# Kernel optimization log

Hardware: AMD Instinct MI355X
Metric: run time of the kernel (lower is better)

## Reference

```python
import jax, jax.numpy as jnp
import numpy as np

N, M, D = 4096, 8192, 512

def setup_inputs() -> dict:
    key = jax.random.key(0)
    k1, k2, k3, k4 = jax.random.split(key, 4)
    X = jax.random.normal(k1, (N, D), dtype=jnp.float32)
    SV = jax.random.normal(k2, (M, D), dtype=jnp.float32)
    DC = jax.random.normal(k3, (1, M), dtype=jnp.float32)
    IC = jax.random.normal(k4, (1,), dtype=jnp.float32)
    gamma = jnp.float32(1.0 / D)
    return {"X": X, "SV": SV, "DC": DC, "IC": IC, "gamma": gamma}

def reference(X, SV, DC, IC, gamma):
    # Squared pairwise L2 distances via GEMM expansion (same math as
    # ||SV - x||^2 without materializing the [N, M, D] broadcast tensor):
    # d2[n, m] = ||x_n||^2 + ||sv_m||^2 - 2 * x_n . sv_m
    x2 = jnp.sum(X * X, axis=1)          # [N]
    sv2 = jnp.sum(SV * SV, axis=1)       # [M]
    cross = jnp.einsum("nd,md->nm", X, SV)  # [N, M]
    d2 = jnp.maximum(x2[:, None] + sv2[None, :] - 2.0 * cross, 0.0)
    k = jnp.exp(-gamma * d2)             # RBF kernel values [N, M]
    # Weighted reduction over support vectors + intercept -> decision values [N]
    return jnp.sum(k * DC, axis=1) + IC
```

## Files before the change

kernel.cpp:

```cpp
#include <hip/hip_runtime.h>
#include <stdint.h>

#define NN 4096
#define MM 8192
#define DD 512
#define KT 8

typedef __bf16 bf16x8 __attribute__((ext_vector_type(8)));
typedef float f32x4 __attribute__((ext_vector_type(4)));
typedef float f32x16 __attribute__((ext_vector_type(16)));

__device__ __forceinline__ void load_lds16(const void* g, void* l) {
  __builtin_amdgcn_global_load_lds(
      (const __attribute__((address_space(1))) unsigned int*)g,
      (__attribute__((address_space(3))) unsigned int*)l, 16, 0, 0);
}

template <int CTRL>
__device__ __forceinline__ float dpp_radd(float x) {
  int xi = __float_as_int(x);
  int mv = __builtin_amdgcn_update_dpp(xi, xi, CTRL, 0xF, 0xF, false);
  return x + __int_as_float(mv);
}
__device__ __forceinline__ float swz_add_xor16(float x) {
  int sv = __builtin_amdgcn_ds_swizzle(__float_as_int(x), 0x401F);
  return x + __int_as_float(sv);
}

__global__ __launch_bounds__(256) void convert_norm_kernel(
    const float* __restrict__ X, const float* __restrict__ SV,
    bf16x8* __restrict__ Xf, bf16x8* __restrict__ SVb,
    float* __restrict__ x2, float* __restrict__ sv2,
    float* __restrict__ out, const float* __restrict__ IC) {
  int wid = blockIdx.x * 4 + (threadIdx.x >> 6);
  int lane = threadIdx.x & 63;
  const float* src;
  float* nrm;
  bool isX = (wid < NN);
  int r = isX ? wid : wid - NN;
  if (isX) {
    src = X + (size_t)r * DD;
    nrm = x2 + r;
    if (lane == 0) out[r] = IC[0];
  } else {
    src = SV + (size_t)r * DD;
    nrm = sv2 + r;
  }
  const f32x4* s = (const f32x4*)src;
  f32x4 a = s[2 * lane];
  f32x4 b = s[2 * lane + 1];
  float sum = a.x * a.x + a.y * a.y + a.z * a.z + a.w * a.w +
              b.x * b.x + b.y * b.y + b.z * b.z + b.w * b.w;
  bf16x8 o;
  o[0] = (__bf16)a.x; o[1] = (__bf16)a.y; o[2] = (__bf16)a.z; o[3] = (__bf16)a.w;
  o[4] = (__bf16)b.x; o[5] = (__bf16)b.y; o[6] = (__bf16)b.z; o[7] = (__bf16)b.w;
  if (isX) {
    const int rg = r >> 5, r31 = r & 31;
    Xf[((size_t)(rg * 32 + (lane >> 1))) * 64 + (lane & 1) * 32 + r31] = o;
  } else {
    SVb[(size_t)r * 64 + lane] = o;
  }
#pragma unroll
  for (int m = 32; m >= 1; m >>= 1) sum += __shfl_xor(sum, m, 64);
  if (lane == 0) *nrm = sum;
}

__global__ __launch_bounds__(256, 4) void rbf_gemm_kernel(
    const bf16x8* __restrict__ Xf, const bf16x8* __restrict__ SVb,
    const float* __restrict__ x2, const float* __restrict__ sv2,
    const float* __restrict__ DC, const float* __restrict__ gamma_p,
    float* __restrict__ out) {
  __shared__ bf16x8 Bs[2][1024];

  const int t = threadIdx.x;
  const int lane = t & 63;
  const int wave = t >> 6;
  const int n0 = blockIdx.x * 128;
  const int m0 = blockIdx.y * 128;

  const int wave_m = wave & 1;
  const int wave_n = wave >> 1;
  const int l31 = lane & 31;
  const int lhi = lane >> 5;

  const int srow = t >> 3;
  const int sslot = t & 7;

  const int rgb = blockIdx.x * 4 + wave_n * 2;
  const bf16x8* a0p = Xf + (size_t)rgb * 2048 + lane;
  const bf16x8* a1p = a0p + 2048;

  f32x16 acc[2][2];
#pragma unroll
  for (int i = 0; i < 2; ++i)
#pragma unroll
    for (int j = 0; j < 2; ++j)
#pragma unroll
      for (int r = 0; r < 16; ++r) acc[i][j][r] = 0.0f;

#pragma unroll
  for (int it = 0; it < 4; ++it) {
    const int c = it * 256 + t;
    const int row = it * 32 + srow;
    const int kg = sslot ^ (row & 7);
    load_lds16(SVb + (size_t)(m0 + row) * 64 + kg, &Bs[0][c]);
  }
  __syncthreads();

#pragma unroll
  for (int kt = 0; kt < KT; ++kt) {
    const int cur = kt & 1;
    const int nxt = cur ^ 1;
    if (kt + 1 < KT) {
#pragma unroll
      for (int it = 0; it < 4; ++it) {
        const int c = it * 256 + t;
        const int row = it * 32 + srow;
        const int kg = sslot ^ (row & 7);
        load_lds16(SVb + (size_t)(m0 + row) * 64 + (kt + 1) * 8 + kg,
                   &Bs[nxt][c]);
      }
    }
#pragma unroll
    for (int ks = 0; ks < 4; ++ks) {
      const int sg = kt * 4 + ks;
      bf16x8 af0 = a0p[(size_t)sg * 64];
      bf16x8 af1 = a1p[(size_t)sg * 64];
      const int kc = ks * 2 + lhi;
      const int sw = kc ^ (l31 & 7);
      const int rb = (wave_m * 64 + l31) * 8;
      bf16x8 bf0 = Bs[cur][rb + sw];
      bf16x8 bf1 = Bs[cur][rb + 256 + sw];
      acc[0][0] = __builtin_amdgcn_mfma_f32_32x32x16_bf16(af0, bf0, acc[0][0], 0, 0, 0);
      acc[0][1] = __builtin_amdgcn_mfma_f32_32x32x16_bf16(af0, bf1, acc[0][1], 0, 0, 0);
      acc[1][0] = __builtin_amdgcn_mfma_f32_32x32x16_bf16(af1, bf0, acc[1][0], 0, 0, 0);
      acc[1][1] = __builtin_amdgcn_mfma_f32_32x32x16_bf16(af1, bf1, acc[1][1], 0, 0, 0);
    }
    __syncthreads();
  }

  const float g = gamma_p[0];
  const float c2 = g * 1.4426950408889634f;

  float sv2v[2], dcv[2];
  const int colb = m0 + wave_m * 64 + l31;
  sv2v[0] = sv2[colb];
  dcv[0] = DC[colb];
  sv2v[1] = sv2[colb + 32];
  dcv[1] = DC[colb + 32];

#pragma unroll
  for (int i = 0; i < 2; ++i) {
    const int rowb = n0 + wave_n * 64 + i * 32 + 4 * lhi;
    float val[16];
#pragma unroll
    for (int g4 = 0; g4 < 4; ++g4) {
      f32x4 xv = *(const f32x4*)(x2 + rowb + 8 * g4);
#pragma unroll
      for (int r2 = 0; r2 < 4; ++r2) {
        const int reg = g4 * 4 + r2;
        float v = 0.0f;
#pragma unroll
        for (int j = 0; j < 2; ++j) {
          float d2 = xv[r2] + sv2v[j] - 2.0f * acc[i][j][reg];
          d2 = fmaxf(d2, 0.0f);
          v += exp2f(-c2 * d2) * dcv[j];
        }
        val[reg] = v;
      }
    }
#pragma unroll
    for (int reg = 0; reg < 16; ++reg) {
      float v = val[reg];
      v = dpp_radd<0x121>(v);
      v = dpp_radd<0x122>(v);
      v = dpp_radd<0x124>(v);
      v = dpp_radd<0x128>(v);
      val[reg] = swz_add_xor16(v);
    }
    if (l31 == 0) {
#pragma unroll
      for (int g4 = 0; g4 < 4; ++g4)
#pragma unroll
        for (int r2 = 0; r2 < 4; ++r2)
          atomicAdd(&out[rowb + 8 * g4 + r2], val[g4 * 4 + r2]);
    }
  }
}

extern "C" void kernel_launch(void* const* d_in, const int* in_sizes, int n_in,
                              void* d_out, int out_size, void* d_ws, size_t ws_size,
                              hipStream_t stream) {
  const float* X = (const float*)d_in[0];
  const float* SV = (const float*)d_in[1];
  const float* DC = (const float*)d_in[2];
  const float* IC = (const float*)d_in[3];
  const float* gamma = (const float*)d_in[4];
  float* out = (float*)d_out;

  char* ws = (char*)d_ws;
  bf16x8* Xf = (bf16x8*)ws;
  bf16x8* SVb = (bf16x8*)(ws + (size_t)NN * DD * 2);
  float* x2 = (float*)(ws + (size_t)(NN + MM) * DD * 2);
  float* sv2 = x2 + NN;

  convert_norm_kernel<<<(NN + MM) / 4, 256, 0, stream>>>(X, SV, Xf, SVb, x2, sv2, out, IC);
  dim3 grid(NN / 128, MM / 128);
  rbf_gemm_kernel<<<grid, 256, 0, stream>>>(Xf, SVb, x2, sv2, DC, gamma, out);
}
```

Baseline: 140.6 us.

## Load SV fragments directly from global in MFMA layout, drop LDS staging

SV is now converted into the same fragment-major layout as X, so each wave loads both MFMA operands straight from global memory with register double-buffering. The LDS tile, swizzle and per-stage barriers are removed. Occupancy hint drops from 4 to 3 blocks to leave room for the extra registers. The cost is that each B fragment is fetched by two waves instead of once per block through LDS, which doubles global/L2 traffic for B.

Result: slower. 150.1 us (+6.8%).

```diff
diff --git a/kernel.cpp b/kernel.cpp
--- a/kernel.cpp
+++ b/kernel.cpp
@@ -4,17 +4,10 @@
 #define NN 4096
 #define MM 8192
 #define DD 512
-#define KT 8
 
 typedef __bf16 bf16x8 __attribute__((ext_vector_type(8)));
 typedef float f32x4 __attribute__((ext_vector_type(4)));
 typedef float f32x16 __attribute__((ext_vector_type(16)));
-
-__device__ __forceinline__ void load_lds16(const void* g, void* l) {
-  __builtin_amdgcn_global_load_lds(
-      (const __attribute__((address_space(1))) unsigned int*)g,
-      (__attribute__((address_space(3))) unsigned int*)l, 16, 0, 0);
-}
 
 template <int CTRL>
 __device__ __forceinline__ float dpp_radd(float x) {
@@ -29,22 +22,25 @@
 
 __global__ __launch_bounds__(256) void convert_norm_kernel(
     const float* __restrict__ X, const float* __restrict__ SV,
-    bf16x8* __restrict__ Xf, bf16x8* __restrict__ SVb,
+    bf16x8* __restrict__ Xf, bf16x8* __restrict__ SVf,
     float* __restrict__ x2, float* __restrict__ sv2,
     float* __restrict__ out, const float* __restrict__ IC) {
   int wid = blockIdx.x * 4 + (threadIdx.x >> 6);
   int lane = threadIdx.x & 63;
   const float* src;
   float* nrm;
+  bf16x8* dstF;
   bool isX = (wid < NN);
   int r = isX ? wid : wid - NN;
   if (isX) {
     src = X + (size_t)r * DD;
     nrm = x2 + r;
+    dstF = Xf;
     if (lane == 0) out[r] = IC[0];
   } else {
     src = SV + (size_t)r * DD;
     nrm = sv2 + r;
+    dstF = SVf;
   }
   const f32x4* s = (const f32x4*)src;
   f32x4 a = s[2 * lane];
@@ -54,24 +50,17 @@
   bf16x8 o;
   o[0] = (__bf16)a.x; o[1] = (__bf16)a.y; o[2] = (__bf16)a.z; o[3] = (__bf16)a.w;
   o[4] = (__bf16)b.x; o[5] = (__bf16)b.y; o[6] = (__bf16)b.z; o[7] = (__bf16)b.w;
-  if (isX) {
-    const int rg = r >> 5, r31 = r & 31;
-    Xf[((size_t)(rg * 32 + (lane >> 1))) * 64 + (lane & 1) * 32 + r31] = o;
-  } else {
-    SVb[(size_t)r * 64 + lane] = o;
-  }
+  dstF[((size_t)((r >> 5) * 32 + (lane >> 1))) * 64 + (lane & 1) * 32 + (r & 31)] = o;
 #pragma unroll
   for (int m = 32; m >= 1; m >>= 1) sum += __shfl_xor(sum, m, 64);
   if (lane == 0) *nrm = sum;
 }
 
-__global__ __launch_bounds__(256, 4) void rbf_gemm_kernel(
-    const bf16x8* __restrict__ Xf, const bf16x8* __restrict__ SVb,
+__global__ __launch_bounds__(256, 3) void rbf_gemm_kernel(
+    const bf16x8* __restrict__ Xf, const bf16x8* __restrict__ SVf,
     const float* __restrict__ x2, const float* __restrict__ sv2,
     const float* __restrict__ DC, const float* __restrict__ gamma_p,
     float* __restrict__ out) {
-  __shared__ bf16x8 Bs[2][1024];
-
   const int t = threadIdx.x;
   const int lane = t & 63;
   const int wave = t >> 6;
@@ -83,12 +72,12 @@
   const int l31 = lane & 31;
   const int lhi = lane >> 5;
 
-  const int srow = t >> 3;
-  const int sslot = t & 7;
-
-  const int rgb = blockIdx.x * 4 + wave_n * 2;
-  const bf16x8* a0p = Xf + (size_t)rgb * 2048 + lane;
-  const bf16x8* a1p = a0p + 2048;
+  const int rgA = blockIdx.x * 4 + wave_n * 2;
+  const int rgB = blockIdx.y * 4 + wave_m * 2;
+  const bf16x8* ap0 = Xf + (size_t)rgA * 2048 + lane;
+  const bf16x8* ap1 = ap0 + 2048;
+  const bf16x8* bp0 = SVf + (size_t)rgB * 2048 + lane;
+  const bf16x8* bp1 = bp0 + 2048;
 
   f32x16 acc[2][2];
 #pragma unroll
@@ -98,45 +87,22 @@
 #pragma unroll
       for (int r = 0; r < 16; ++r) acc[i][j][r] = 0.0f;
 
+  bf16x8 a0 = ap0[0], a1 = ap1[0], b0 = bp0[0], b1 = bp1[0];
 #pragma unroll
-  for (int it = 0; it < 4; ++it) {
-    const int c = it * 256 + t;
-    const int row = it * 32 + srow;
-    const int kg = sslot ^ (row & 7);
-    load_lds16(SVb + (size_t)(m0 + row) * 64 + kg, &Bs[0][c]);
-  }
-  __syncthreads();
-
-#pragma unroll
-  for (int kt = 0; kt < KT; ++kt) {
-    const int cur = kt & 1;
-    const int nxt = cur ^ 1;
-    if (kt + 1 < KT) {
-#pragma unroll
-      for (int it = 0; it < 4; ++it) {
-        const int c = it * 256 + t;
-        const int row = it * 32 + srow;
-        const int kg = sslot ^ (row & 7);
-        load_lds16(SVb + (size_t)(m0 + row) * 64 + (kt + 1) * 8 + kg,
-                   &Bs[nxt][c]);
-      }
+  for (int sg = 0; sg < 32; ++sg) {
+    bf16x8 na0, na1, nb0, nb1;
+    if (sg + 1 < 32) {
+      const size_t o = (size_t)(sg + 1) * 64;
+      na0 = ap0[o];
+      na1 = ap1[o];
+      nb0 = bp0[o];
+      nb1 = bp1[o];
     }
-#pragma unroll
-    for (int ks = 0; ks < 4; ++ks) {
-      const int sg = kt * 4 + ks;
-      bf16x8 af0 = a0p[(size_t)sg * 64];
-      bf16x8 af1 = a1p[(size_t)sg * 64];
-      const int kc = ks * 2 + lhi;
-      const int sw = kc ^ (l31 & 7);
-      const int rb = (wave_m * 64 + l31) * 8;
-      bf16x8 bf0 = Bs[cur][rb + sw];
-      bf16x8 bf1 = Bs[cur][rb + 256 + sw];
-      acc[0][0] = __builtin_amdgcn_mfma_f32_32x32x16_bf16(af0, bf0, acc[0][0], 0, 0, 0);
-      acc[0][1] = __builtin_amdgcn_mfma_f32_32x32x16_bf16(af0, bf1, acc[0][1], 0, 0, 0);
-      acc[1][0] = __builtin_amdgcn_mfma_f32_32x32x16_bf16(af1, bf0, acc[1][0], 0, 0, 0);
-      acc[1][1] = __builtin_amdgcn_mfma_f32_32x32x16_bf16(af1, bf1, acc[1][1], 0, 0, 0);
-    }
-    __syncthreads();
+    acc[0][0] = __builtin_amdgcn_mfma_f32_32x32x16_bf16(a0, b0, acc[0][0], 0, 0, 0);
+    acc[0][1] = __builtin_amdgcn_mfma_f32_32x32x16_bf16(a0, b1, acc[0][1], 0, 0, 0);
+    acc[1][0] = __builtin_amdgcn_mfma_f32_32x32x16_bf16(a1, b0, acc[1][0], 0, 0, 0);
+    acc[1][1] = __builtin_amdgcn_mfma_f32_32x32x16_bf16(a1, b1, acc[1][1], 0, 0, 0);
+    a0 = na0; a1 = na1; b0 = nb0; b1 = nb1;
   }
 
   const float g = gamma_p[0];
@@ -200,11 +166,11 @@
 
   char* ws = (char*)d_ws;
   bf16x8* Xf = (bf16x8*)ws;
-  bf16x8* SVb = (bf16x8*)(ws + (size_t)NN * DD * 2);
+  bf16x8* SVf = (bf16x8*)(ws + (size_t)NN * DD * 2);
   float* x2 = (float*)(ws + (size_t)(NN + MM) * DD * 2);
   float* sv2 = x2 + NN;
 
-  convert_norm_kernel<<<(NN + MM) / 4, 256, 0, stream>>>(X, SV, Xf, SVb, x2, sv2, out, IC);
+  convert_norm_kernel<<<(NN + MM) / 4, 256, 0, stream>>>(X, SV, Xf, SVf, x2, sv2, out, IC);
   dim3 grid(NN / 128, MM / 128);
-  rbf_gemm_kernel<<<grid, 256, 0, stream>>>(Xf, SVb, x2, sv2, DC, gamma, out);
+  rbf_gemm_kernel<<<grid, 256, 0, stream>>>(Xf, SVf, x2, sv2, DC, gamma, out);
 }
```
